# Kernel optimization log

Hardware: AMD Instinct MI355X
Metric: run time of the kernel (lower is better)

## Reference

```python
import jax, jax.numpy as jnp
import numpy as np

S, B, M, F, C = 32, 128, 128, 512, 100


def setup_inputs() -> dict:
    key = jax.random.key(0)
    k = jax.random.split(key, 7)
    x = jax.random.normal(k[0], (B, F), dtype=jnp.float32)
    y = jax.random.randint(k[1], (B,), 0, C, dtype=jnp.int32)
    # Z in {-1, +1}: Bernoulli(0.5) sample mapped via 2*b - 1 (mirrors sample_Z)
    Zb = (jax.random.uniform(k[2], (S, B, M)) < 0.5).astype(jnp.float32)
    Z = 2.0 * Zb - 1.0
    alpha_0 = jax.random.normal(k[3], (M,), dtype=jnp.float32)
    init_c = 2.0 / np.sqrt(F)
    alpha = init_c * jax.random.normal(k[4], (M, F), dtype=jnp.float32)
    alpha = alpha / jnp.linalg.norm(alpha, axis=0, keepdims=True)
    beta_0 = jax.random.normal(k[5], (C,), dtype=jnp.float32)
    init_c2 = 2.0 / np.sqrt(M)
    beta = init_c2 * jax.random.normal(k[6], (C, M), dtype=jnp.float32)
    return {"x": x, "y": y, "Z": Z, "alpha_0": alpha_0, "alpha": alpha,
            "beta_0": beta_0, "beta": beta}


def reference(x, y, Z, alpha_0, alpha, beta_0, beta):
    # linear_eta / eta (compute_linear_eta, compute_eta)
    linear_eta = alpha_0[None, :] + x @ alpha.T            # [B, M]
    eta = jax.nn.sigmoid(linear_eta)                        # exp(l)/(1+exp(l))

    y_onehot = jax.nn.one_hot(y, C, dtype=Z.dtype)          # [B, C]
    # Unperturbed logits shared across all j (rank-1 structure of compute_pi_j)
    base = beta_0[None, None, :] + jnp.einsum('sbm,cm->sbc', Z, beta)  # [S,B,C]

    def pi_for(target):
        # Flipping column j of Z to `target` shifts logits by (target - Z_j)*beta[:, j]
        delta = (target - Z)[..., None] * beta.T[None, None, :, :]  # [S,B,M,C]
        lin = base[:, :, None, :] + delta                            # [S,B,M,C]
        # NOTE: original ADDS the max (faithful to source); softmax ratio unchanged
        lin = lin + jnp.max(lin, axis=-1, keepdims=True)
        num = jnp.sum(y_onehot[None, :, None, :] * lin, axis=-1)     # [S,B,M]
        den = jnp.sum(jnp.exp(lin), axis=-1)                         # [S,B,M]
        return jnp.exp(num) / den                                    # [S,B,M]

    pi_pos = pi_for(1.0)
    pi_neg = pi_for(-1.0)
    # compute_EY_X_j: sum over Monte-Carlo samples
    EY_X_j = jnp.sum(pi_pos * eta[None] + pi_neg * (1.0 - eta)[None], axis=0)  # [B,M]
    return EY_X_j
```

## Files before the change

### kernel.cpp

```cpp
#include <hip/hip_runtime.h>
#include <math.h>

#define S_ 32
#define B_ 128
#define M_ 128
#define F_ 512
#define C_ 100

typedef _Float16 f16;
typedef _Float16 f16x8 __attribute__((ext_vector_type(8)));
typedef float f32x4 __attribute__((ext_vector_type(4)));

__global__ __launch_bounds__(512) void k_all(
    const float* __restrict__ x, const int* __restrict__ y,
    const float* __restrict__ Z, const float* __restrict__ alpha0,
    const float* __restrict__ alpha, const float* __restrict__ beta0,
    const float* __restrict__ beta, float* __restrict__ out) {
  const int mh = blockIdx.x;
  const int b = blockIdx.y;
  const int tid = threadIdx.x;
  const int lane = tid & 63;
  const int w = tid >> 6;
  const int l15 = lane & 15;
  const int lg = lane >> 4;

  __shared__ __align__(16) f16 ZAf[512 * 8];
  __shared__ __align__(16) f16 PtAf[512 * 8];
  __shared__ float baseS[S_ * 112];
  __shared__ float PybS[S_];
  __shared__ float etaS[64];
  __shared__ float redS[128];

  const int yb = y[b];

  {
    int s = tid;
    int kcs = s >> 7, rts = (s >> 6) & 1;
    int lgs = (s >> 4) & 3, l15s = s & 15;
    int p = rts * 16 + l15s;
    int m0 = kcs * 32 + lgs * 8;
    const float* zrow = Z + ((size_t)p * B_ + b) * M_ + m0;
    float4 u0 = *(const float4*)zrow;
    float4 u1 = *(const float4*)(zrow + 4);
    f16x8 hv = {(f16)u0.x, (f16)u0.y, (f16)u0.z, (f16)u0.w,
                (f16)u1.x, (f16)u1.y, (f16)u1.z, (f16)u1.w};
    *(f16x8*)&ZAf[s * 8] = hv;
  }

  {
    const float4* x4 = (const float4*)x;
    const float4* a4 = (const float4*)alpha;
    float4 xr[8];
#pragma unroll
    for (int r = 0; r < 8; ++r) xr[r] = x4[b * 128 + r * 16 + l15];
#pragma unroll
    for (int j = 0; j < 2; ++j) {
      int ml = w * 8 + j * 4 + lg;
      int m = mh * 64 + ml;
      float acc = 0.f;
#pragma unroll
      for (int r = 0; r < 8; ++r) {
        float4 av = a4[(size_t)m * 128 + r * 16 + l15];
        float4 xv = xr[r];
        acc = fmaf(av.x, xv.x, acc); acc = fmaf(av.y, xv.y, acc);
        acc = fmaf(av.z, xv.z, acc); acc = fmaf(av.w, xv.w, acc);
      }
      acc += __shfl_xor(acc, 1);
      acc += __shfl_xor(acc, 2);
      acc += __shfl_xor(acc, 4);
      acc += __shfl_xor(acc, 8);
      if (l15 == 0) {
        float l = alpha0[m] + acc;
        etaS[ml] = 1.f / (1.f + __expf(-l));
      }
    }
  }

  const int colB = w * 16 + l15;
  f16x8 bfr[4];
  if (w < 7) {
    const float* brow = beta + (size_t)((colB < C_) ? colB : C_ - 1) * M_;
    bool ok = colB < C_;
#pragma unroll
    for (int kc = 0; kc < 4; ++kc) {
      int m0 = kc * 32 + lg * 8;
      float4 u0 = *(const float4*)(brow + m0);
      float4 u1 = *(const float4*)(brow + m0 + 4);
      if (!ok) { u0 = make_float4(0,0,0,0); u1 = make_float4(0,0,0,0); }
      bfr[kc] = (f16x8){(f16)u0.x, (f16)u0.y, (f16)u0.z, (f16)u0.w,
                        (f16)u1.x, (f16)u1.y, (f16)u1.z, (f16)u1.w};
    }
  }

  const int pt = w >> 2, mt = w & 3;
  const int mD = mh * 64 + mt * 16 + l15;
  f16x8 bp[4], bn[4];
  {
    const float* bcol = beta + mD;
#pragma unroll
    for (int kc = 0; kc < 4; ++kc) {
      f16x8 ep, en;
#pragma unroll
      for (int ii = 0; ii < 8; ++ii) {
        int c = kc * 32 + lg * 8 + ii;
        int cs = (c < C_) ? c : C_ - 1;
        float bv = bcol[(size_t)cs * M_];
        float e = __expf(2.f * bv);
        ep[ii] = (f16)e;
        en[ii] = (f16)(1.f / e);
      }
      bp[kc] = ep;
      bn[kc] = en;
    }
  }
  __syncthreads();

  if (w < 7) {
    f32x4 acc0 = {0.f, 0.f, 0.f, 0.f}, acc1 = {0.f, 0.f, 0.f, 0.f};
#pragma unroll
    for (int kc = 0; kc < 4; ++kc) {
      f16x8 a0 = *(const f16x8*)&ZAf[((kc * 2 + 0) * 64 + lane) * 8];
      f16x8 a1 = *(const f16x8*)&ZAf[((kc * 2 + 1) * 64 + lane) * 8];
      acc0 = __builtin_amdgcn_mfma_f32_16x16x32_f16(a0, bfr[kc], acc0, 0, 0, 0);
      acc1 = __builtin_amdgcn_mfma_f32_16x16x32_f16(a1, bfr[kc], acc1, 0, 0, 0);
    }
    float b0v = (colB < C_) ? beta0[colB] : 0.f;
#pragma unroll
    for (int j = 0; j < 4; ++j) {
      baseS[(lg * 4 + j) * 112 + colB] = acc0[j] + b0v;
      baseS[(16 + lg * 4 + j) * 112 + colB] = acc1[j] + b0v;
    }
  }
  __syncthreads();

  {
#pragma unroll
    for (int k = 0; k < 4; ++k) {
      int p = w * 4 + k;
      float v1 = baseS[p * 112 + lane];
      float v2 = (lane < 36) ? baseS[p * 112 + 64 + lane] : -1e30f;
      float mx = fmaxf(v1, v2);
#pragma unroll
      for (int off = 32; off > 0; off >>= 1) mx = fmaxf(mx, __shfl_xor(mx, off));
      float e1 = __expf(v1 - mx);
      float e2 = (lane < 36) ? __expf(v2 - mx) : 0.f;
      float sm = e1 + e2;
#pragma unroll
      for (int off = 32; off > 0; off >>= 1) sm += __shfl_xor(sm, off);
      float rd = 1.f / sm;
      float p1 = e1 * rd;
      float p2 = (lane < 36) ? e2 * rd : 0.f;
      int ptp = p >> 4, l15p = p & 15;
      {
        int c = lane, kc = c >> 5, lg2 = (c >> 3) & 3, ii = c & 7;
        PtAf[((kc * 2 + ptp) * 64 + lg2 * 16 + l15p) * 8 + ii] = (f16)p1;
      }
      {
        int c = lane + 64, kc = c >> 5, lg2 = (c >> 3) & 3, ii = c & 7;
        PtAf[((kc * 2 + ptp) * 64 + lg2 * 16 + l15p) * 8 + ii] = (f16)p2;
      }
      if (lane == yb) PybS[p] = p1;
      if (lane + 64 == yb) PybS[p] = p2;
    }
  }
  __syncthreads();

  {
    f32x4 pA = {0.f, 0.f, 0.f, 0.f}, nA = {0.f, 0.f, 0.f, 0.f};
#pragma unroll
    for (int kc = 0; kc < 4; ++kc) {
      f16x8 a0 = *(const f16x8*)&PtAf[((kc * 2 + pt) * 64 + lane) * 8];
      pA = __builtin_amdgcn_mfma_f32_16x16x32_f16(a0, bp[kc], pA, 0, 0, 0);
      nA = __builtin_amdgcn_mfma_f32_16x16x32_f16(a0, bn[kc], nA, 0, 0, 0);
    }
    int m = mD;
    float bym = beta[yb * M_ + m];
    float epy = __expf(2.f * bym), eny = 1.f / epy;
    float eta_v = etaS[mt * 16 + l15];
    float ome = 1.f - eta_v;
    float o = 0.f;
    int kcz = m >> 5, lgz = (m >> 3) & 3, iiz = m & 7;
#pragma unroll
    for (int j = 0; j < 4; ++j) {
      int p = pt * 16 + lg * 4 + j;
      float z = (float)ZAf[((kcz * 2 + (p >> 4)) * 64 + lgz * 16 + (p & 15)) * 8 + iiz];
      float pyb = PybS[p];
      o += (z > 0.f) ? fmaf(pyb, eta_v, (pyb * eny / nA[j]) * ome)
                     : fmaf(pyb * epy / pA[j], eta_v, pyb * ome);
    }
    o += __shfl_xor(o, 16);
    o += __shfl_xor(o, 32);
    if (lane < 16) redS[pt * 64 + mt * 16 + l15] = o;
  }
  __syncthreads();

  if (tid < 64) out[b * M_ + mh * 64 + tid] = redS[tid] + redS[64 + tid];
}

extern "C" void kernel_launch(void* const* d_in, const int* in_sizes, int n_in,
                              void* d_out, int out_size, void* d_ws, size_t ws_size,
                              hipStream_t stream) {
  const float* x = (const float*)d_in[0];
  const int* y = (const int*)d_in[1];
  const float* Z = (const float*)d_in[2];
  const float* alpha0 = (const float*)d_in[3];
  const float* alpha = (const float*)d_in[4];
  const float* beta0 = (const float*)d_in[5];
  const float* beta = (const float*)d_in[6];
  float* out = (float*)d_out;

  k_all<<<dim3(2, B_), dim3(512), 0, stream>>>(x, y, Z, alpha0, alpha, beta0,
                                               beta, out);
}
```

Baseline: 16.18 us.

## Split M across four blocks per batch row with split-K MFMA reduction

Doubles the grid from 2 to 4 blocks per batch row, so each block handles 32 M columns instead of 64. The final pi MFMA stage is split along K across wave pairs, with the partial accumulators combined through shared memory and an extra barrier. This is meant to spread work over more CUs on a 256-CU part. In exchange, each block still recomputes the shared base logits GEMM and softmax, so that redundant work doubles overall.

After: 18.71 us. +15.6%, slower.

```diff
diff --git a/kernel.cpp b/kernel.cpp
--- a/kernel.cpp
+++ b/kernel.cpp
@@ -16,7 +16,7 @@
     const float* __restrict__ Z, const float* __restrict__ alpha0,
     const float* __restrict__ alpha, const float* __restrict__ beta0,
     const float* __restrict__ beta, float* __restrict__ out) {
-  const int mh = blockIdx.x;
+  const int mq = blockIdx.x;
   const int b = blockIdx.y;
   const int tid = threadIdx.x;
   const int lane = tid & 63;
@@ -27,9 +27,10 @@
   __shared__ __align__(16) f16 ZAf[512 * 8];
   __shared__ __align__(16) f16 PtAf[512 * 8];
   __shared__ float baseS[S_ * 112];
+  __shared__ __align__(16) float pnS[4 * 2 * 64 * 4];
   __shared__ float PybS[S_];
-  __shared__ float etaS[64];
-  __shared__ float redS[128];
+  __shared__ float etaS[32];
+  __shared__ float redS[64];
 
   const int yb = y[b];
 
@@ -53,26 +54,23 @@
     float4 xr[8];
 #pragma unroll
     for (int r = 0; r < 8; ++r) xr[r] = x4[b * 128 + r * 16 + l15];
-#pragma unroll
-    for (int j = 0; j < 2; ++j) {
-      int ml = w * 8 + j * 4 + lg;
-      int m = mh * 64 + ml;
-      float acc = 0.f;
-#pragma unroll
-      for (int r = 0; r < 8; ++r) {
-        float4 av = a4[(size_t)m * 128 + r * 16 + l15];
-        float4 xv = xr[r];
-        acc = fmaf(av.x, xv.x, acc); acc = fmaf(av.y, xv.y, acc);
-        acc = fmaf(av.z, xv.z, acc); acc = fmaf(av.w, xv.w, acc);
-      }
-      acc += __shfl_xor(acc, 1);
-      acc += __shfl_xor(acc, 2);
-      acc += __shfl_xor(acc, 4);
-      acc += __shfl_xor(acc, 8);
-      if (l15 == 0) {
-        float l = alpha0[m] + acc;
-        etaS[ml] = 1.f / (1.f + __expf(-l));
-      }
+    int ml = w * 4 + lg;
+    int m = mq * 32 + ml;
+    float acc = 0.f;
+#pragma unroll
+    for (int r = 0; r < 8; ++r) {
+      float4 av = a4[(size_t)m * 128 + r * 16 + l15];
+      float4 xv = xr[r];
+      acc = fmaf(av.x, xv.x, acc); acc = fmaf(av.y, xv.y, acc);
+      acc = fmaf(av.z, xv.z, acc); acc = fmaf(av.w, xv.w, acc);
+    }
+    acc += __shfl_xor(acc, 1);
+    acc += __shfl_xor(acc, 2);
+    acc += __shfl_xor(acc, 4);
+    acc += __shfl_xor(acc, 8);
+    if (l15 == 0) {
+      float l = alpha0[m] + acc;
+      etaS[ml] = 1.f / (1.f + __expf(-l));
     }
   }
 
@@ -92,13 +90,14 @@
     }
   }
 
-  const int pt = w >> 2, mt = w & 3;
-  const int mD = mh * 64 + mt * 16 + l15;
-  f16x8 bp[4], bn[4];
+  const int pt = (w >> 2) & 1, mt = (w >> 1) & 1, kh = w & 1;
+  const int mD = mq * 32 + mt * 16 + l15;
+  f16x8 bp[2], bn[2];
   {
     const float* bcol = beta + mD;
 #pragma unroll
-    for (int kc = 0; kc < 4; ++kc) {
+    for (int t = 0; t < 2; ++t) {
+      int kc = kh * 2 + t;
       f16x8 ep, en;
 #pragma unroll
       for (int ii = 0; ii < 8; ++ii) {
@@ -109,8 +108,8 @@
         ep[ii] = (f16)e;
         en[ii] = (f16)(1.f / e);
       }
-      bp[kc] = ep;
-      bn[kc] = en;
+      bp[t] = ep;
+      bn[t] = en;
     }
   }
   __syncthreads();
@@ -165,14 +164,30 @@
   }
   __syncthreads();
 
-  {
-    f32x4 pA = {0.f, 0.f, 0.f, 0.f}, nA = {0.f, 0.f, 0.f, 0.f};
-#pragma unroll
-    for (int kc = 0; kc < 4; ++kc) {
-      f16x8 a0 = *(const f16x8*)&PtAf[((kc * 2 + pt) * 64 + lane) * 8];
-      pA = __builtin_amdgcn_mfma_f32_16x16x32_f16(a0, bp[kc], pA, 0, 0, 0);
-      nA = __builtin_amdgcn_mfma_f32_16x16x32_f16(a0, bn[kc], nA, 0, 0, 0);
-    }
+  f32x4 pA = {0.f, 0.f, 0.f, 0.f}, nA = {0.f, 0.f, 0.f, 0.f};
+#pragma unroll
+  for (int t = 0; t < 2; ++t) {
+    int kc = kh * 2 + t;
+    f16x8 a0 = *(const f16x8*)&PtAf[((kc * 2 + pt) * 64 + lane) * 8];
+    pA = __builtin_amdgcn_mfma_f32_16x16x32_f16(a0, bp[t], pA, 0, 0, 0);
+    nA = __builtin_amdgcn_mfma_f32_16x16x32_f16(a0, bn[t], nA, 0, 0, 0);
+  }
+  {
+    int tile = pt * 2 + mt;
+    if (kh == 1) {
+      *(f32x4*)&pnS[((tile * 2 + 0) * 64 + lane) * 4] = pA;
+      *(f32x4*)&pnS[((tile * 2 + 1) * 64 + lane) * 4] = nA;
+    }
+  }
+  __syncthreads();
+
+  if (kh == 0) {
+    int tile = pt * 2 + mt;
+    f32x4 pB = *(const f32x4*)&pnS[((tile * 2 + 0) * 64 + lane) * 4];
+    f32x4 nB = *(const f32x4*)&pnS[((tile * 2 + 1) * 64 + lane) * 4];
+#pragma unroll
+    for (int j = 0; j < 4; ++j) { pA[j] += pB[j]; nA[j] += nB[j]; }
+
     int m = mD;
     float bym = beta[yb * M_ + m];
     float epy = __expf(2.f * bym), eny = 1.f / epy;
@@ -190,11 +205,11 @@
     }
     o += __shfl_xor(o, 16);
     o += __shfl_xor(o, 32);
-    if (lane < 16) redS[pt * 64 + mt * 16 + l15] = o;
-  }
-  __syncthreads();
-
-  if (tid < 64) out[b * M_ + mh * 64 + tid] = redS[tid] + redS[64 + tid];
+    if (lane < 16) redS[pt * 32 + mt * 16 + l15] = o;
+  }
+  __syncthreads();
+
+  if (tid < 32) out[b * M_ + mq * 32 + tid] = redS[tid] + redS[32 + tid];
 }
 
 extern "C" void kernel_launch(void* const* d_in, const int* in_sizes, int n_in,
@@ -209,6 +224,6 @@
   const float* beta = (const float*)d_in[6];
   float* out = (float*)d_out;
 
-  k_all<<<dim3(2, B_), dim3(512), 0, stream>>>(x, y, Z, alpha0, alpha, beta0,
+  k_all<<<dim3(4, B_), dim3(512), 0, stream>>>(x, y, Z, alpha0, alpha, beta0,
                                                beta, out);
 }
```
